# Optimization experiments

Measured on AMD Instinct MI355X. Metric: run time of the kernel, lower is better.

## Reference

```python
import jax, jax.numpy as jnp
import numpy as np

B, S, H, NH, KVH, HD = 8, 4096, 4096, 32, 8, 128
STEP = 2048
EPS = 1e-6


def _rotate_half(x):
    x1, x2 = x[..., : HD // 2], x[..., HD // 2 :]
    return jnp.concatenate([-x2, x1], axis=-1)


def _rmsnorm(x, w):
    xf = x.astype(jnp.float32)
    var = jnp.mean(xf * xf, axis=-1, keepdims=True)
    return w * (xf * jax.lax.rsqrt(var + EPS)).astype(x.dtype)


def setup_inputs() -> dict:
    key = jax.random.key(0)
    ks = jax.random.split(key, 10)
    wscale = 0.02
    hidden_states = jax.random.normal(ks[0], (B, 1, H), jnp.float32)
    # RoPE angles for position STEP
    inv_freq = 1.0 / (10000.0 ** (jnp.arange(0, HD, 2, dtype=jnp.float32) / HD))
    ang = STEP * inv_freq  # [HD/2]
    emb = jnp.concatenate([ang, ang])  # [HD]
    cos = jnp.broadcast_to(jnp.cos(emb), (B, 1, HD)).astype(jnp.float32)
    sin = jnp.broadcast_to(jnp.sin(emb), (B, 1, HD)).astype(jnp.float32)
    key_cache = jax.random.normal(ks[1], (B, KVH, S, HD), jnp.float32)
    value_cache = jax.random.normal(ks[2], (B, KVH, S, HD), jnp.float32)
    # additive causal mask: rows 0..STEP, cols 0..S-1; -1e9 where col > row
    rows = jnp.arange(STEP + 1)[:, None]
    cols = jnp.arange(S)[None, :]
    causal_mask = jnp.where(cols <= rows, 0.0, -1e9).astype(jnp.float32)[None, None]
    q_w = jax.random.normal(ks[3], (H, NH * HD), jnp.float32) * wscale
    k_w = jax.random.normal(ks[4], (H, KVH * HD), jnp.float32) * wscale
    v_w = jax.random.normal(ks[5], (H, KVH * HD), jnp.float32) * wscale
    o_w = jax.random.normal(ks[6], (NH * HD, H), jnp.float32) * wscale
    q_norm_w = jnp.ones((HD,), jnp.float32)
    k_norm_w = jnp.ones((HD,), jnp.float32)
    return {
        "hidden_states": hidden_states, "cos": cos, "sin": sin,
        "key_cache": key_cache, "value_cache": value_cache,
        "causal_mask": causal_mask, "q_w": q_w, "k_w": k_w, "v_w": v_w,
        "o_w": o_w, "q_norm_w": q_norm_w, "k_norm_w": k_norm_w,
        "step_idx": STEP,
    }


def reference(hidden_states, cos, sin, key_cache, value_cache, causal_mask,
              q_w, k_w, v_w, o_w, q_norm_w, k_norm_w, step_idx):
    G = NH // KVH
    scaling = HD ** -0.5
    bsz = hidden_states.shape[0]
    # projections + QK-RMSNorm; (B,1,nH,HD) -> (B,nH,1,HD)
    q = _rmsnorm((hidden_states @ q_w).reshape(bsz, 1, NH, HD), q_norm_w).transpose(0, 2, 1, 3)
    k = _rmsnorm((hidden_states @ k_w).reshape(bsz, 1, KVH, HD), k_norm_w).transpose(0, 2, 1, 3)
    v = (hidden_states @ v_w).reshape(bsz, 1, KVH, HD).transpose(0, 2, 1, 3)
    # RoPE (cos/sin broadcast over head axis)
    c = cos[:, None, :, :]  # (B,1,1,HD)
    s = sin[:, None, :, :]
    q = q * c + _rotate_half(q) * s
    k = k * c + _rotate_half(k) * s
    # single-step cache write
    key_cache = key_cache.at[:, :, step_idx : step_idx + 1].set(k)
    value_cache = value_cache.at[:, :, step_idx : step_idx + 1].set(v)
    # GQA attention without materializing repeat_kv (same math)
    qg = q.reshape(bsz, KVH, G, 1, HD)
    scores = jnp.einsum("bkgqd,bksd->bkgqs", qg, key_cache) * scaling  # (B,KVH,G,1,S)
    scores = scores.reshape(bsz, NH, 1, S) + causal_mask[:, :, step_idx : step_idx + 1, :]
    attn = jax.nn.softmax(scores.astype(jnp.float32), axis=-1).astype(q.dtype)
    out = jnp.einsum("bkgqs,bksd->bkgqd", attn.reshape(bsz, KVH, G, 1, S), value_cache)
    out = out.reshape(bsz, NH, 1, HD).transpose(0, 2, 1, 3).reshape(bsz, 1, NH * HD)
    return out @ o_w
```

## Files before the change

### kernel.cpp

```cpp
#include <hip/hip_runtime.h>
#include <math.h>

#define Bq 8
#define Sq 4096
#define Hq 4096
#define NHq 32
#define KVHq 8
#define HDq 128
#define QKV_N 6144
#define CHUNK 256
#define NCHUNK 16
#define ROWS 128

__global__ __launch_bounds__(256) void gemv_splitk(
    const float* __restrict__ x, const float* __restrict__ W,
    float* __restrict__ y, int K, int ldW, int ldY) {
  __shared__ float xs[Bq][ROWS];
  int tid = threadIdx.x;
  int r0 = blockIdx.y * ROWS;
  for (int i = tid; i < Bq * ROWS; i += 256) {
    int b = i >> 7, r = i & (ROWS - 1);
    xs[b][r] = x[b * K + r0 + r];
  }
  __syncthreads();
  int col = blockIdx.x * 256 + tid;
  float acc[Bq] = {0, 0, 0, 0, 0, 0, 0, 0};
  const float* wp = W + (size_t)r0 * ldW + col;
  for (int r = 0; r < ROWS; r += 16) {
    float w[16];
#pragma unroll
    for (int j = 0; j < 16; j++) w[j] = wp[(size_t)j * ldW];
    wp += (size_t)16 * ldW;
#pragma unroll
    for (int b = 0; b < Bq; b++) {
      float4 x0 = *(const float4*)&xs[b][r];
      float4 x1 = *(const float4*)&xs[b][r + 4];
      float4 x2 = *(const float4*)&xs[b][r + 8];
      float4 x3 = *(const float4*)&xs[b][r + 12];
      acc[b] = fmaf(x0.x, w[0], acc[b]);
      acc[b] = fmaf(x0.y, w[1], acc[b]);
      acc[b] = fmaf(x0.z, w[2], acc[b]);
      acc[b] = fmaf(x0.w, w[3], acc[b]);
      acc[b] = fmaf(x1.x, w[4], acc[b]);
      acc[b] = fmaf(x1.y, w[5], acc[b]);
      acc[b] = fmaf(x1.z, w[6], acc[b]);
      acc[b] = fmaf(x1.w, w[7], acc[b]);
      acc[b] = fmaf(x2.x, w[8], acc[b]);
      acc[b] = fmaf(x2.y, w[9], acc[b]);
      acc[b] = fmaf(x2.z, w[10], acc[b]);
      acc[b] = fmaf(x2.w, w[11], acc[b]);
      acc[b] = fmaf(x3.x, w[12], acc[b]);
      acc[b] = fmaf(x3.y, w[13], acc[b]);
      acc[b] = fmaf(x3.z, w[14], acc[b]);
      acc[b] = fmaf(x3.w, w[15], acc[b]);
    }
  }
#pragma unroll
  for (int b = 0; b < Bq; b++) atomicAdd(&y[b * ldY + col], acc[b]);
}

__global__ __launch_bounds__(256) void gemv_fused_qkv(
    const float* __restrict__ x, const float* __restrict__ qw,
    const float* __restrict__ kw, const float* __restrict__ vw,
    float* __restrict__ y) {
  __shared__ float xs[Bq][ROWS];
  int tid = threadIdx.x;
  int r0 = blockIdx.y * ROWS;
  for (int i = tid; i < Bq * ROWS; i += 256) {
    int b = i >> 7, r = i & (ROWS - 1);
    xs[b][r] = x[b * Hq + r0 + r];
  }
  __syncthreads();
  int col = blockIdx.x * 256 + tid;
  const float* W;
  int ldW, wcol;
  if (col < NHq * HDq) { W = qw; ldW = NHq * HDq; wcol = col; }
  else if (col < NHq * HDq + KVHq * HDq) { W = kw; ldW = KVHq * HDq; wcol = col - NHq * HDq; }
  else { W = vw; ldW = KVHq * HDq; wcol = col - (NHq + KVHq) * HDq; }
  float acc[Bq] = {0, 0, 0, 0, 0, 0, 0, 0};
  const float* wp = W + (size_t)r0 * ldW + wcol;
  for (int r = 0; r < ROWS; r += 16) {
    float w[16];
#pragma unroll
    for (int j = 0; j < 16; j++) w[j] = wp[(size_t)j * ldW];
    wp += (size_t)16 * ldW;
#pragma unroll
    for (int b = 0; b < Bq; b++) {
      float4 x0 = *(const float4*)&xs[b][r];
      float4 x1 = *(const float4*)&xs[b][r + 4];
      float4 x2 = *(const float4*)&xs[b][r + 8];
      float4 x3 = *(const float4*)&xs[b][r + 12];
      acc[b] = fmaf(x0.x, w[0], acc[b]);
      acc[b] = fmaf(x0.y, w[1], acc[b]);
      acc[b] = fmaf(x0.z, w[2], acc[b]);
      acc[b] = fmaf(x0.w, w[3], acc[b]);
      acc[b] = fmaf(x1.x, w[4], acc[b]);
      acc[b] = fmaf(x1.y, w[5], acc[b]);
      acc[b] = fmaf(x1.z, w[6], acc[b]);
      acc[b] = fmaf(x1.w, w[7], acc[b]);
      acc[b] = fmaf(x2.x, w[8], acc[b]);
      acc[b] = fmaf(x2.y, w[9], acc[b]);
      acc[b] = fmaf(x2.z, w[10], acc[b]);
      acc[b] = fmaf(x2.w, w[11], acc[b]);
      acc[b] = fmaf(x3.x, w[12], acc[b]);
      acc[b] = fmaf(x3.y, w[13], acc[b]);
      acc[b] = fmaf(x3.z, w[14], acc[b]);
      acc[b] = fmaf(x3.w, w[15], acc[b]);
    }
  }
#pragma unroll
  for (int b = 0; b < Bq; b++) atomicAdd(&y[b * QKV_N + col], acc[b]);
}

__global__ __launch_bounds__(256) void normrope(
    const float* __restrict__ qkv, const float* __restrict__ cosp,
    const float* __restrict__ sinp, const float* __restrict__ qnw,
    const float* __restrict__ knw, const int* __restrict__ step_ptr,
    float* __restrict__ kcache, float* __restrict__ vcache,
    float* __restrict__ qvec) {
  int tid = threadIdx.x;
  int lane = tid & 63, wid = tid >> 6;
  int vec = blockIdx.x * 4 + wid;
  int step = *step_ptr;
  if (vec < 256) {
    int b = vec >> 5, h = vec & 31;
    const float* src = qkv + b * QKV_N + h * HDq;
    float x0 = src[lane], x1 = src[lane + 64];
    float ss = fmaf(x0, x0, x1 * x1);
#pragma unroll
    for (int off = 32; off; off >>= 1) ss += __shfl_xor(ss, off, 64);
    float sc = rsqrtf(ss * (1.0f / HDq) + 1e-6f);
    float n0 = x0 * sc * qnw[lane], n1 = x1 * sc * qnw[lane + 64];
    float c0 = cosp[b * HDq + lane], c1 = cosp[b * HDq + lane + 64];
    float s0 = sinp[b * HDq + lane], s1 = sinp[b * HDq + lane + 64];
    float* dst = qvec + b * (NHq * HDq) + h * HDq;
    dst[lane] = fmaf(n0, c0, -n1 * s0);
    dst[lane + 64] = fmaf(n1, c1, n0 * s1);
  } else if (vec < 320) {
    int v = vec - 256;
    int b = v >> 3, kvh = v & 7;
    const float* src = qkv + b * QKV_N + NHq * HDq + kvh * HDq;
    float x0 = src[lane], x1 = src[lane + 64];
    float ss = fmaf(x0, x0, x1 * x1);
#pragma unroll
    for (int off = 32; off; off >>= 1) ss += __shfl_xor(ss, off, 64);
    float sc = rsqrtf(ss * (1.0f / HDq) + 1e-6f);
    float n0 = x0 * sc * knw[lane], n1 = x1 * sc * knw[lane + 64];
    float c0 = cosp[b * HDq + lane], c1 = cosp[b * HDq + lane + 64];
    float s0 = sinp[b * HDq + lane], s1 = sinp[b * HDq + lane + 64];
    float* dst = kcache + (((size_t)(b * KVHq + kvh)) * Sq + step) * HDq;
    dst[lane] = fmaf(n0, c0, -n1 * s0);
    dst[lane + 64] = fmaf(n1, c1, n0 * s1);
  } else {
    int v = vec - 320;
    int b = v >> 3, kvh = v & 7;
    const float* src = qkv + b * QKV_N + (NHq + KVHq) * HDq + kvh * HDq;
    float* dst = vcache + (((size_t)(b * KVHq + kvh)) * Sq + step) * HDq;
    dst[lane] = src[lane];
    dst[lane + 64] = src[lane + 64];
  }
}

__global__ __launch_bounds__(256) void attn_partial(
    const float* __restrict__ qvec, const float* __restrict__ kc,
    const float* __restrict__ vc, const int* __restrict__ step_ptr,
    float* __restrict__ pm, float* __restrict__ pl, float* __restrict__ po) {
  int c = blockIdx.x;
  int bk = blockIdx.y;
  int b = bk >> 3, kvh = bk & 7;
  int step = *step_ptr;
  int base = c * CHUNK;
  int pidx = (bk * NCHUNK + c) * 4;
  int tid = threadIdx.x;
  if (base > step) {
    if (tid < 4) { pm[pidx + tid] = -1e38f; pl[pidx + tid] = 0.0f; }
    return;
  }
  __shared__ float qs[4][HDq];
  __shared__ float red[4][4];
  __shared__ float pls[4][CHUNK];
  __shared__ float ored[2][4][HDq];
  for (int i = tid; i < 4 * HDq; i += 256)
    qs[i >> 7][i & 127] = qvec[b * (NHq * HDq) + (kvh * 4 + (i >> 7)) * HDq + (i & 127)];
  __syncthreads();

  int s = base + tid;
  const float* krow = kc + (((size_t)bk) * Sq + s) * HDq;
  float sc[4] = {0, 0, 0, 0};
#pragma unroll 8
  for (int d = 0; d < HDq; d += 4) {
    float4 kk = *(const float4*)(krow + d);
#pragma unroll
    for (int g = 0; g < 4; g++) {
      float4 qq = *(const float4*)&qs[g][d];
      sc[g] += kk.x * qq.x + kk.y * qq.y + kk.z * qq.z + kk.w * qq.w;
    }
  }
  const float scaling = 0.08838834764831845f;
  bool valid = (s <= step);
#pragma unroll
  for (int g = 0; g < 4; g++) sc[g] = valid ? sc[g] * scaling : -1e30f;

  int lane = tid & 63, wid = tid >> 6;
#pragma unroll
  for (int g = 0; g < 4; g++) {
    float v = sc[g];
#pragma unroll
    for (int off = 32; off; off >>= 1) v = fmaxf(v, __shfl_xor(v, off, 64));
    if (lane == 0) red[g][wid] = v;
  }
  __syncthreads();
  float m[4];
#pragma unroll
  for (int g = 0; g < 4; g++)
    m[g] = fmaxf(fmaxf(red[g][0], red[g][1]), fmaxf(red[g][2], red[g][3]));
  __syncthreads();
#pragma unroll
  for (int g = 0; g < 4; g++) {
    float p = __expf(sc[g] - m[g]);
    pls[g][tid] = p;
    float v = p;
#pragma unroll
    for (int off = 32; off; off >>= 1) v += __shfl_xor(v, off, 64);
    if (lane == 0) red[g][wid] = v;
  }
  __syncthreads();
  if (tid < 4) {
    pm[pidx + tid] = m[tid];
    pl[pidx + tid] = red[tid][0] + red[tid][1] + red[tid][2] + red[tid][3];
  }
  int d = tid & 127, h = tid >> 7;
  const float* vb = vc + (((size_t)bk) * Sq + base + h * (CHUNK / 2)) * HDq + d;
  float o[4] = {0, 0, 0, 0};
#pragma unroll 4
  for (int ss = 0; ss < CHUNK / 2; ss += 4) {
    float vv0 = vb[(size_t)(ss + 0) * HDq];
    float vv1 = vb[(size_t)(ss + 1) * HDq];
    float vv2 = vb[(size_t)(ss + 2) * HDq];
    float vv3 = vb[(size_t)(ss + 3) * HDq];
#pragma unroll
    for (int g = 0; g < 4; g++) {
      float4 p = *(const float4*)&pls[g][h * (CHUNK / 2) + ss];
      o[g] = fmaf(p.x, vv0, o[g]);
      o[g] = fmaf(p.y, vv1, o[g]);
      o[g] = fmaf(p.z, vv2, o[g]);
      o[g] = fmaf(p.w, vv3, o[g]);
    }
  }
#pragma unroll
  for (int g = 0; g < 4; g++) ored[h][g][d] = o[g];
  __syncthreads();
  if (h == 0) {
#pragma unroll
    for (int g = 0; g < 4; g++)
      po[(size_t)(pidx + g) * HDq + d] = ored[0][g][d] + ored[1][g][d];
  }
}

__global__ __launch_bounds__(128) void attn_combine(
    const float* __restrict__ pm, const float* __restrict__ pl,
    const float* __restrict__ po, float* __restrict__ aout) {
  int bh = blockIdx.x;
  int b = bh >> 5, h = bh & 31;
  int kvh = h >> 2, g = h & 3;
  int d = threadIdx.x;
  int bk = b * KVHq + kvh;
  float mv[NCHUNK];
  float M = -1e38f;
#pragma unroll
  for (int c = 0; c < NCHUNK; c++) {
    mv[c] = pm[(bk * NCHUNK + c) * 4 + g];
    M = fmaxf(M, mv[c]);
  }
  float L = 0.0f, o = 0.0f;
#pragma unroll
  for (int c = 0; c < NCHUNK; c++) {
    if (mv[c] > -1e37f) {
      float w = __expf(mv[c] - M);
      L = fmaf(pl[(bk * NCHUNK + c) * 4 + g], w, L);
      o = fmaf(po[(size_t)((bk * NCHUNK + c) * 4 + g) * HDq + d], w, o);
    }
  }
  aout[b * (NHq * HDq) + h * HDq + d] = o / L;
}

extern "C" void kernel_launch(void* const* d_in, const int* in_sizes, int n_in,
                              void* d_out, int out_size, void* d_ws, size_t ws_size,
                              hipStream_t stream) {
  const float* hidden = (const float*)d_in[0];
  const float* cosp   = (const float*)d_in[1];
  const float* sinp   = (const float*)d_in[2];
  float* kcache       = (float*)d_in[3];
  float* vcache       = (float*)d_in[4];
  const float* q_w    = (const float*)d_in[6];
  const float* k_w    = (const float*)d_in[7];
  const float* v_w    = (const float*)d_in[8];
  const float* o_w    = (const float*)d_in[9];
  const float* qnw    = (const float*)d_in[10];
  const float* knw    = (const float*)d_in[11];
  const int* step_ptr = (const int*)d_in[12];
  float* out = (float*)d_out;
  float* ws = (float*)d_ws;

  float* qkv  = ws;
  float* qvec = ws + 49152;
  float* aout = ws + 81920;
  float* pm   = ws + 114688;
  float* pl   = ws + 118784;
  float* po   = ws + 122880;
  (void)in_sizes; (void)n_in; (void)ws_size;

  (void)hipMemsetAsync(qkv, 0, 49152 * sizeof(float), stream);
  (void)hipMemsetAsync(out, 0, (size_t)out_size * sizeof(float), stream);

  gemv_fused_qkv<<<dim3(QKV_N / 256, Hq / ROWS), 256, 0, stream>>>(hidden, q_w, k_w, v_w, qkv);

  normrope<<<96, 256, 0, stream>>>(qkv, cosp, sinp, qnw, knw, step_ptr, kcache, vcache, qvec);

  attn_partial<<<dim3(NCHUNK, Bq * KVHq), 256, 0, stream>>>(qvec, kcache, vcache, step_ptr, pm, pl, po);
  attn_combine<<<Bq * NHq, 128, 0, stream>>>(pm, pl, po, aout);

  gemv_splitk<<<dim3(16, Hq / ROWS), 256, 0, stream>>>(aout, o_w, out, NHq * HDq, 4096, 4096);
}
```

Measured before the change: 428.0 us.

## Vectorize V loads, prefetch V before softmax, and batch K loads in attention partial

```diff
diff --git a/kernel.cpp b/kernel.cpp
--- a/kernel.cpp
+++ b/kernel.cpp
@@ -179,7 +179,7 @@
   __shared__ float qs[4][HDq];
   __shared__ float red[4][4];
   __shared__ float pls[4][CHUNK];
-  __shared__ float ored[2][4][HDq];
+  __shared__ float4 ored[8][4][32];
   for (int i = tid; i < 4 * HDq; i += 256)
     qs[i >> 7][i & 127] = qvec[b * (NHq * HDq) + (kvh * 4 + (i >> 7)) * HDq + (i & 127)];
   __syncthreads();
@@ -187,19 +187,33 @@
   int s = base + tid;
   const float* krow = kc + (((size_t)bk) * Sq + s) * HDq;
   float sc[4] = {0, 0, 0, 0};
-#pragma unroll 8
-  for (int d = 0; d < HDq; d += 4) {
-    float4 kk = *(const float4*)(krow + d);
-#pragma unroll
-    for (int g = 0; g < 4; g++) {
-      float4 qq = *(const float4*)&qs[g][d];
-      sc[g] += kk.x * qq.x + kk.y * qq.y + kk.z * qq.z + kk.w * qq.w;
+#pragma unroll
+  for (int dd = 0; dd < HDq; dd += 64) {
+    float4 kk[16];
+#pragma unroll
+    for (int j = 0; j < 16; j++) kk[j] = *(const float4*)(krow + dd + j * 4);
+#pragma unroll
+    for (int j = 0; j < 16; j++) {
+#pragma unroll
+      for (int g = 0; g < 4; g++) {
+        float4 qq = *(const float4*)&qs[g][dd + j * 4];
+        sc[g] = fmaf(kk[j].x, qq.x, sc[g]);
+        sc[g] = fmaf(kk[j].y, qq.y, sc[g]);
+        sc[g] = fmaf(kk[j].z, qq.z, sc[g]);
+        sc[g] = fmaf(kk[j].w, qq.w, sc[g]);
+      }
     }
   }
   const float scaling = 0.08838834764831845f;
   bool valid = (s <= step);
 #pragma unroll
   for (int g = 0; g < 4; g++) sc[g] = valid ? sc[g] * scaling : -1e30f;
+
+  int q4 = tid & 31, grp = tid >> 5;
+  const float* vb = vc + (((size_t)bk) * Sq + base + grp * 32) * HDq + q4 * 4;
+  float4 vpre[8];
+#pragma unroll
+  for (int j = 0; j < 8; j++) vpre[j] = *(const float4*)(vb + (size_t)j * HDq);
 
   int lane = tid & 63, wid = tid >> 6;
 #pragma unroll
@@ -229,31 +243,49 @@
     pm[pidx + tid] = m[tid];
     pl[pidx + tid] = red[tid][0] + red[tid][1] + red[tid][2] + red[tid][3];
   }
-  int d = tid & 127, h = tid >> 7;
-  const float* vb = vc + (((size_t)bk) * Sq + base + h * (CHUNK / 2)) * HDq + d;
-  float o[4] = {0, 0, 0, 0};
-#pragma unroll 4
-  for (int ss = 0; ss < CHUNK / 2; ss += 4) {
-    float vv0 = vb[(size_t)(ss + 0) * HDq];
-    float vv1 = vb[(size_t)(ss + 1) * HDq];
-    float vv2 = vb[(size_t)(ss + 2) * HDq];
-    float vv3 = vb[(size_t)(ss + 3) * HDq];
+
+  float4 o[4];
+#pragma unroll
+  for (int g = 0; g < 4; g++) { o[g].x = 0; o[g].y = 0; o[g].z = 0; o[g].w = 0; }
+#pragma unroll
+  for (int j = 0; j < 8; j++) {
 #pragma unroll
     for (int g = 0; g < 4; g++) {
-      float4 p = *(const float4*)&pls[g][h * (CHUNK / 2) + ss];
-      o[g] = fmaf(p.x, vv0, o[g]);
-      o[g] = fmaf(p.y, vv1, o[g]);
-      o[g] = fmaf(p.z, vv2, o[g]);
-      o[g] = fmaf(p.w, vv3, o[g]);
-    }
-  }
-#pragma unroll
-  for (int g = 0; g < 4; g++) ored[h][g][d] = o[g];
-  __syncthreads();
-  if (h == 0) {
-#pragma unroll
-    for (int g = 0; g < 4; g++)
-      po[(size_t)(pidx + g) * HDq + d] = ored[0][g][d] + ored[1][g][d];
+      float p = pls[g][grp * 32 + j];
+      o[g].x = fmaf(p, vpre[j].x, o[g].x);
+      o[g].y = fmaf(p, vpre[j].y, o[g].y);
+      o[g].z = fmaf(p, vpre[j].z, o[g].z);
+      o[g].w = fmaf(p, vpre[j].w, o[g].w);
+    }
+  }
+  for (int ss = 8; ss < 32; ss += 8) {
+    float4 vv[8];
+#pragma unroll
+    for (int j = 0; j < 8; j++) vv[j] = *(const float4*)(vb + (size_t)(ss + j) * HDq);
+#pragma unroll
+    for (int j = 0; j < 8; j++) {
+#pragma unroll
+      for (int g = 0; g < 4; g++) {
+        float p = pls[g][grp * 32 + ss + j];
+        o[g].x = fmaf(p, vv[j].x, o[g].x);
+        o[g].y = fmaf(p, vv[j].y, o[g].y);
+        o[g].z = fmaf(p, vv[j].z, o[g].z);
+        o[g].w = fmaf(p, vv[j].w, o[g].w);
+      }
+    }
+  }
+#pragma unroll
+  for (int g = 0; g < 4; g++) ored[grp][g][q4] = o[g];
+  __syncthreads();
+  if (tid < 128) {
+    int g = tid >> 5, q = tid & 31;
+    float4 sum = ored[0][g][q];
+#pragma unroll
+    for (int r = 1; r < 8; r++) {
+      float4 t = ored[r][g][q];
+      sum.x += t.x; sum.y += t.y; sum.z += t.z; sum.w += t.w;
+    }
+    *(float4*)&po[(size_t)(pidx + g) * HDq + q * 4] = sum;
   }
 }
 
```

Measured after the change: 452.9 us. +5.8%, slower.
